# Optimization experiments

Hardware: AMD Instinct MI355X
Metric: run time of the kernel (lower is better)

## Reference

```python
import jax, jax.numpy as jnp
import numpy as np

N_SEEDS = 2500
N_JOINTS = 24
D_FEAT = 131


def setup_inputs() -> dict:
    key = jax.random.key(0)
    k1, k2, k3, k4, k5 = jax.random.split(key, 5)
    B = 256
    seed_features = jax.random.normal(k1, (B, N_SEEDS, D_FEAT), dtype=jnp.float32)
    # Conv1d kernel_size=1 weights == matrices over the channel dim
    s1 = 1.0 / np.sqrt(N_SEEDS)
    s2 = 1.0 / np.sqrt(N_JOINTS)
    W1 = jax.random.uniform(k2, (N_JOINTS, N_SEEDS), jnp.float32, -s1, s1)
    b1 = jax.random.uniform(k3, (N_JOINTS,), jnp.float32, -s1, s1)
    W2 = jax.random.uniform(k4, (N_JOINTS, N_JOINTS), jnp.float32, -s2, s2)
    b2 = jax.random.uniform(k5, (N_JOINTS,), jnp.float32, -s2, s2)
    return {"seed_features": seed_features, "W1": W1, "b1": b1, "W2": W2, "b2": b2}


def reference(seed_features, W1, b1, W2, b2):
    # conv1d(k=1) over channels: [B,2500,131] -> [B,24,131]
    h = jax.nn.relu(jnp.einsum('oc,bcl->bol', W1, seed_features) + b1[None, :, None])
    query = jnp.einsum('oc,bcl->bol', W2, h) + b2[None, :, None]        # [B,24,131]
    scores = jnp.einsum('bjl,bnl->bjn', query, seed_features)            # [B,24,2500]
    attention = jax.nn.softmax(scores, axis=-1)
    output = jnp.einsum('bjn,bnl->bjl', attention, seed_features)        # [B,24,131]
    return output, attention
```

## Files before the change

### kernel.cpp

```cpp
#include <hip/hip_runtime.h>
#include <cstdint>
#include <cstddef>

#define NB 256
#define NS 2500
#define NJ 24
#define DF 131

#define QSEG 4
#define TSEG 640

#define KP 2528
#define XROWS 2528
#define LPq 136
#define CSP 66
#define OSTRIDE ((size_t)NB * NJ * DF)

using short8 = __attribute__((ext_vector_type(8))) short;
using f32x4  = __attribute__((ext_vector_type(4))) float;

#define F_XN   0ull
#define F_W1B  176029696ull
#define F_QBF  176191488ull
#define F_PO   178419712ull
#define F_MD   191297536ull
#define F_P    191494144ull
#define WS_FULL 222558208ull

__device__ __forceinline__ unsigned short f2bf(float x) {
  union { float f; unsigned u; } v; v.f = x;
  unsigned r = v.u + 0x7fffu + ((v.u >> 16) & 1u);
  return (unsigned short)(r >> 16);
}
__device__ __forceinline__ float bf2f(unsigned us) {
  union { unsigned u; float f; } v; v.u = us << 16;
  return v.f;
}
__device__ __forceinline__ f32x4 mfma16(short8 a, short8 b, f32x4 c) {
  return __builtin_amdgcn_mfma_f32_16x16x32_bf16(a, b, c, 0, 0, 0);
}

__global__ __launch_bounds__(256) void kT2(const float* __restrict__ W1,
                                           unsigned short* __restrict__ W1b) {
  int dwi = blockIdx.x * 256 + threadIdx.x;
  if (dwi >= 32 * (KP / 2)) return;
  int row = dwi / (KP / 2);
  int kk = (dwi - row * (KP / 2)) * 2;
  unsigned lo = (row < NJ && kk     < NS) ? f2bf(W1[row * NS + kk])     : 0;
  unsigned hi = (row < NJ && kk + 1 < NS) ? f2bf(W1[row * NS + kk + 1]) : 0;
  ((unsigned*)W1b)[dwi] = lo | (hi << 16);
}

__global__ __launch_bounds__(256) void kPn(const float* __restrict__ sf,
                                           unsigned short* __restrict__ Xn) {
  int b = blockIdx.x / 20;
  int chunk = blockIdx.x - 20 * b;
  int c0 = chunk * 128;
  int w = threadIdx.x >> 6, lane = threadIdx.x & 63;
  const float* xb = sf + (size_t)b * (NS * DF);
  unsigned short* xnb = Xn + (size_t)b * ((size_t)XROWS * LPq);

#pragma unroll 4
  for (int i = 0; i < 32; ++i) {
    int r = w * 32 + i;
    int c = c0 + r;
    if (c >= XROWS) continue;
    bool vc = c < NS;
    const float* g = xb + (size_t)c * DF;
    float v0 = vc ? g[lane] : 0.f;
    float v1 = vc ? g[64 + lane] : 0.f;
    float v2 = (vc && lane < 3) ? g[128 + lane] : 0.f;
    unsigned short* d = xnb + (size_t)c * LPq;
    d[lane] = f2bf(v0);
    d[64 + lane] = f2bf(v1);
    if (lane < 8) d[128 + lane] = (lane < 3) ? f2bf(v2) : (unsigned short)0;
  }
}

__global__ __launch_bounds__(512) void kMM(const unsigned short* __restrict__ Xn,
                                           const unsigned short* __restrict__ A,
                                           int astride, int amax,
                                           float* __restrict__ Cp) {
  __shared__ unsigned short xs[144 * CSP];
  unsigned* xs4 = (unsigned*)xs;
  int b = blockIdx.x >> 2;
  int s = blockIdx.x & 3;
  int w = threadIdx.x >> 6, lane = threadIdx.x & 63;
  int lr = lane & 15, lg = lane >> 4;
  const unsigned* xb4 = (const unsigned*)(Xn + (size_t)b * ((size_t)XROWS * LPq));
  const unsigned short* Ab = A + (size_t)b * astride * KP;

  int nu = (w < 2) ? 3 : 2;
  f32x4 acc[3];
#pragma unroll
  for (int t = 0; t < 3; ++t) acc[t] = (f32x4){0.f, 0.f, 0.f, 0.f};

  int ch0 = s * 10;
  unsigned pre[9];
#pragma unroll
  for (int k = 0; k < 8; ++k)
    pre[k] = xb4[(size_t)(ch0 * 64 + w * 8 + k) * (LPq / 2) + lane];
  pre[8] = 0;
  if (lane < 32)
    pre[8] = xb4[(size_t)(ch0 * 64 + w * 8 + (lane >> 2)) * (LPq / 2) + 64 + (lane & 3)];

  for (int i = 0; i < 10; ++i) {
    int ch = ch0 + i;
    int c0 = ch * 64;
    int CS = (ch < 39) ? 64 : 32;
    __syncthreads();
#pragma unroll
    for (int k = 0; k < 8; ++k) {
      int r = w * 8 + k;
      if (r < CS) {
        xs[(2 * lane) * CSP + r]     = (unsigned short)(pre[k] & 0xffffu);
        xs[(2 * lane + 1) * CSP + r] = (unsigned short)(pre[k] >> 16);
      }
    }
    if (lane < 32) {
      int r = w * 8 + (lane >> 2);
      if (r < CS) {
        int l0 = 128 + 2 * (lane & 3);
        xs[l0 * CSP + r]       = (unsigned short)(pre[8] & 0xffffu);
        xs[(l0 + 1) * CSP + r] = (unsigned short)(pre[8] >> 16);
      }
    }
    __syncthreads();
    if (i + 1 < 10) {
      int c1 = c0 + 64;
      int CSn = (ch + 1 < 39) ? 64 : 32;
#pragma unroll
      for (int k = 0; k < 8; ++k) {
        int r = w * 8 + k;
        pre[k] = (r < CSn) ? xb4[(size_t)(c1 + r) * (LPq / 2) + lane] : 0u;
      }
      pre[8] = 0;
      if (lane < 32) {
        int r = w * 8 + (lane >> 2);
        if (r < CSn)
          pre[8] = xb4[(size_t)(c1 + r) * (LPq / 2) + 64 + (lane & 3)];
      }
    }
    int nks = CS >> 5;
    for (int ks = 0; ks < nks; ++ks) {
#pragma unroll
      for (int t = 0; t < 3; ++t) {
        if (t < nu) {
          int u = w + 8 * t;
          int m = u / 9, nt = u - 9 * m;
          int arow = m * 16 + lr; if (arow > amax) arow = amax;
          const unsigned short* ap = Ab + (size_t)arow * KP + c0 + ks * 32 + lg * 8;
          short8 av = *(const short8*)ap;
          int bb = (nt * 16 + lr) * (CSP / 2) + ks * 16 + lg * 4;
          unsigned b0 = xs4[bb], b1 = xs4[bb + 1], b2 = xs4[bb + 2], b3 = xs4[bb + 3];
          short8 bv;
          ((unsigned*)&bv)[0] = b0; ((unsigned*)&bv)[1] = b1;
          ((unsigned*)&bv)[2] = b2; ((unsigned*)&bv)[3] = b3;
          acc[t] = mfma16(av, bv, acc[t]);
        }
      }
    }
  }
  float* Cb = Cp + (size_t)(s * NB + b) * (NJ * DF);
#pragma unroll
  for (int t = 0; t < 3; ++t) {
    if (t < nu) {
      int u = w + 8 * t;
      int m = u / 9, nt = u - 9 * m;
      int lcol = nt * 16 + lr;
      if (lcol < DF) {
#pragma unroll
        for (int r = 0; r < 4; ++r) {
          int j = m * 16 + lg * 4 + r;
          if (j < NJ) Cb[(size_t)j * DF + lcol] = acc[t][r];
        }
      }
    }
  }
}

__global__ __launch_bounds__(512) void kR4(const float* __restrict__ po,
                                           float* __restrict__ out) {
  int i = blockIdx.x * 512 + threadIdx.x;
  out[i] = po[i] + po[OSTRIDE + i] + po[2 * OSTRIDE + i] + po[3 * OSTRIDE + i];
}

__global__ __launch_bounds__(512) void k1b(const float* __restrict__ po,
                                           const float* __restrict__ W2,
                                           const float* __restrict__ b1v,
                                           const float* __restrict__ b2v,
                                           unsigned short* __restrict__ qbf) {
  int flat = blockIdx.x * 512 + threadIdx.x;
  if (flat >= NB * LPq) return;
  int l = flat % LPq;
  int b = flat / LPq;
  unsigned short* qp = qbf + (size_t)b * (32 * LPq) + l;
  if (l >= DF) {
#pragma unroll
    for (int j = 0; j < 32; ++j) qp[j * LPq] = 0;
    return;
  }
  const float* p0 = po + (size_t)b * (NJ * DF) + l;
  float hv[NJ];
#pragma unroll
  for (int o = 0; o < NJ; ++o)
    hv[o] = fmaxf(b1v[o] + p0[o * DF] + p0[OSTRIDE + o * DF] +
                  p0[2 * OSTRIDE + o * DF] + p0[3 * OSTRIDE + o * DF], 0.f);
  float q[NJ];
  for (int o = 0; o < NJ; ++o) {
    float sv = b2v[o];
#pragma unroll
    for (int i = 0; i < NJ; ++i) sv = fmaf(W2[o * NJ + i], hv[i], sv);
    q[o] = sv;
  }
#pragma unroll
  for (int j = 0; j < NJ; ++j) qp[j * LPq] = f2bf(q[j]);
#pragma unroll
  for (int j = NJ; j < 32; ++j) qp[j * LPq] = 0;
}

__global__ __launch_bounds__(512) void k2m(const unsigned short* __restrict__ Xn,
                                           const unsigned short* __restrict__ qbf,
                                           unsigned short* __restrict__ P,
                                           float* __restrict__ md) {
  __shared__ float wm[8][24];
  __shared__ float wd[8][24];
  int b = blockIdx.x >> 2, seg = blockIdx.x & 3;
  int w = threadIdx.x >> 6, lane = threadIdx.x & 63;
  int lr = lane & 15, lg = lane >> 4;
  const short8 z8 = {0, 0, 0, 0, 0, 0, 0, 0};

  const unsigned short* qb = qbf + (size_t)b * (32 * LPq);
  short8 aq0[5], aq1[5];
#pragma unroll
  for (int ks = 0; ks < 4; ++ks) {
    aq0[ks] = *(const short8*)(qb + (size_t)lr * LPq + ks * 32 + lg * 8);
    aq1[ks] = *(const short8*)(qb + (size_t)(16 + lr) * LPq + ks * 32 + lg * 8);
  }
  aq0[4] = (lg == 0) ? *(const short8*)(qb + (size_t)lr * LPq + 128) : z8;
  aq1[4] = (lg == 0) ? *(const short8*)(qb + (size_t)(16 + lr) * LPq + 128) : z8;

  const unsigned short* xb = Xn + (size_t)b * ((size_t)XROWS * LPq);
  int ntl = (seg < 3) ? 40 : 37;

  f32x4 s0[5], s1[5];
  float m8[8];
#pragma unroll
  for (int r = 0; r < 8; ++r) m8[r] = -1e30f;

#pragma unroll
  for (int i = 0; i < 5; ++i) {
    s0[i] = (f32x4){0.f, 0.f, 0.f, 0.f};
    s1[i] = (f32x4){0.f, 0.f, 0.f, 0.f};
    int ti = w + 8 * i;
    if (ti < ntl) {
      int n = (seg * 40 + ti) * 16 + lr;
      const unsigned short* bp = xb + (size_t)n * LPq + lg * 8;
      short8 bx[5];
#pragma unroll
      for (int ks = 0; ks < 4; ++ks) bx[ks] = *(const short8*)(bp + ks * 32);
      bx[4] = (lg == 0) ? *(const short8*)(xb + (size_t)n * LPq + 128) : z8;
      f32x4 a0 = {0.f, 0.f, 0.f, 0.f}, a1 = {0.f, 0.f, 0.f, 0.f};
#pragma unroll
      for (int ks = 0; ks < 5; ++ks) {
        a0 = mfma16(aq0[ks], bx[ks], a0);
        a1 = mfma16(aq1[ks], bx[ks], a1);
      }
      s0[i] = a0; s1[i] = a1;
#pragma unroll
      for (int r = 0; r < 4; ++r) {
        m8[r]     = fmaxf(m8[r],     a0[r]);
        m8[4 + r] = fmaxf(m8[4 + r], a1[r]);
      }
    }
  }
#pragma unroll
  for (int r = 0; r < 8; ++r)
#pragma unroll
    for (int off = 1; off < 16; off <<= 1)
      m8[r] = fmaxf(m8[r], __shfl_xor(m8[r], off));
  if (lr == 0) {
#pragma unroll
    for (int r = 0; r < 4; ++r) {
      wm[w][lg * 4 + r] = m8[r];
      if (lg < 2) wm[w][16 + lg * 4 + r] = m8[4 + r];
    }
  }
  __syncthreads();
  float mseg[8];
#pragma unroll
  for (int r = 0; r < 4; ++r) {
    float m0 = wm[0][lg * 4 + r];
#pragma unroll
    for (int wv = 1; wv < 8; ++wv) m0 = fmaxf(m0, wm[wv][lg * 4 + r]);
    mseg[r] = m0;
    int j1 = 16 + (lg & 1) * 4 + r;
    float m1 = wm[0][j1];
#pragma unroll
    for (int wv = 1; wv < 8; ++wv) m1 = fmaxf(m1, wm[wv][j1]);
    mseg[4 + r] = m1;
  }
  float d8[8];
#pragma unroll
  for (int r = 0; r < 8; ++r) d8[r] = 0.f;
#pragma unroll
  for (int i = 0; i < 5; ++i) {
    int ti = w + 8 * i;
    if (ti < ntl) {
      int n = (seg * 40 + ti) * 16 + lr;
      bool valid = n < NS;
#pragma unroll
      for (int r = 0; r < 4; ++r) {
        float p0 = __expf(s0[i][r] - mseg[r]);
        float p1 = __expf(s1[i][r] - mseg[4 + r]);
        if (valid) {
          P[((size_t)b * NJ + lg * 4 + r) * KP + n] = f2bf(p0);
          d8[r] += p0;
          if (lg < 2) {
            P[((size_t)b * NJ + 16 + lg * 4 + r) * KP + n] = f2bf(p1);
            d8[4 + r] += p1;
          }
        }
      }
    }
  }
#pragma unroll
  for (int r = 0; r < 8; ++r)
#pragma unroll
    for (int off = 1; off < 16; off <<= 1)
      d8[r] += __shfl_xor(d8[r], off);
  if (lr == 0) {
#pragma unroll
    for (int r = 0; r < 4; ++r) {
      wd[w][lg * 4 + r] = d8[r];
      if (lg < 2) wd[w][16 + lg * 4 + r] = d8[4 + r];
    }
  }
  __syncthreads();
  if (threadIdx.x < NJ) {
    int j = threadIdx.x;
    float m = wm[0][j], d = 0.f;
#pragma unroll
    for (int wv = 1; wv < 8; ++wv) m = fmaxf(m, wm[wv][j]);
#pragma unroll
    for (int wv = 0; wv < 8; ++wv) d += wd[wv][j];
    float* mp = md + ((size_t)b * QSEG + seg) * 48;
    mp[j] = m;
    mp[24 + j] = d;
  }
}

__global__ __launch_bounds__(256) void kW(unsigned short* __restrict__ P,
                                          const float* __restrict__ md,
                                          float* __restrict__ attn) {
  int bj = blockIdx.x;
  int b = bj / NJ, j = bj - b * NJ;
  const float* mp = md + (size_t)b * (QSEG * 48);
  float ms[QSEG];
  float m = -1e30f;
#pragma unroll
  for (int s = 0; s < QSEG; ++s) { ms[s] = mp[s * 48 + j]; m = fmaxf(m, ms[s]); }
  float d = 0.f;
#pragma unroll
  for (int s = 0; s < QSEG; ++s) d += mp[s * 48 + 24 + j] * __expf(ms[s] - m);
  float rinv = 1.f / d;
  float cs[QSEG];
#pragma unroll
  for (int s = 0; s < QSEG; ++s) cs[s] = __expf(ms[s] - m) * rinv;

  unsigned* prow = (unsigned*)(P + (size_t)bj * KP);
  float2* arow = (float2*)(attn + (size_t)bj * NS);
  for (int i = threadIdx.x; i < NS / 2; i += 256) {
    unsigned pk = prow[i];
    int n0 = 2 * i;
    float p0 = bf2f(pk & 0xffffu) * cs[n0 / TSEG];
    float p1 = bf2f(pk >> 16) * cs[(n0 + 1) / TSEG];
    arow[i] = make_float2(p0, p1);
    prow[i] = (unsigned)f2bf(p0) | ((unsigned)f2bf(p1) << 16);
  }
  if (threadIdx.x < (KP - NS) / 2) prow[NS / 2 + threadIdx.x] = 0;
}

#define KSEG 8
#define CSEG 313
#define SEGN 625
#define TN 64
#define LDP 132
#define WS_W1T 0u
#define WS_QTF 60000u
#define WS_MDF (WS_QTF + 804864u)
#define WS_PHF (WS_MDF + (unsigned)(NB * QSEG * 48))
#define SEGSTRIDE ((size_t)NB * NJ * DF)

__global__ __launch_bounds__(256) void kT_f(const float* __restrict__ W1,
                                            float* __restrict__ W1t) {
  int i = blockIdx.x * 256 + threadIdx.x;
  if (i >= NJ * NS) return;
  int o = i / NS, c = i - o * NS;
  W1t[c * NJ + o] = W1[i];
}

__global__ __launch_bounds__(192) void kH_f(const float* __restrict__ sf,
                                            const float* __restrict__ W1t,
                                            float* __restrict__ ph) {
  int b = blockIdx.x >> 3;
  int s = blockIdx.x & 7;
  int l = threadIdx.x;
  int c0 = s * CSEG;
  int cnt = NS - c0; if (cnt > CSEG) cnt = CSEG;
  const float* xp = sf + (size_t)b * (NS * DF) + (size_t)c0 * DF;
  const float* wp = W1t + (size_t)c0 * NJ;
  float acc[NJ];
#pragma unroll
  for (int o = 0; o < NJ; ++o) acc[o] = 0.f;
  if (l < DF) {
#pragma unroll 2
    for (int c = 0; c < cnt; ++c) {
      float xv = xp[(size_t)c * DF + l];
#pragma unroll
      for (int o = 0; o < NJ; ++o) acc[o] = fmaf(wp[c * NJ + o], xv, acc[o]);
    }
    float* pp = ph + (size_t)(s * NB + b) * (NJ * DF) + l;
#pragma unroll
    for (int o = 0; o < NJ; ++o) pp[o * DF] = acc[o];
  }
}

__global__ __launch_bounds__(512) void k1b_f(const float* __restrict__ ph,
                                             const float* __restrict__ W2,
                                             const float* __restrict__ b1v,
                                             const float* __restrict__ b2v,
                                             float* __restrict__ q_t) {
  int flat = blockIdx.x * 512 + threadIdx.x;
  if (flat >= NB * DF) return;
  int l = flat % DF;
  int b = flat / DF;
  const float* p0 = ph + (size_t)(b * NJ) * DF + l;
  float hv[NJ];
#pragma unroll
  for (int o = 0; o < NJ; ++o) hv[o] = b1v[o];
  for (int s = 0; s < KSEG; ++s) {
#pragma unroll
    for (int o = 0; o < NJ; ++o) hv[o] += p0[s * SEGSTRIDE + o * DF];
  }
#pragma unroll
  for (int o = 0; o < NJ; ++o) hv[o] = fmaxf(hv[o], 0.f);
  float q[NJ];
  for (int o = 0; o < NJ; ++o) {
    float sv = b2v[o];
#pragma unroll
    for (int i = 0; i < NJ; ++i) sv = fmaf(W2[o * NJ + i], hv[i], sv);
    q[o] = sv;
  }
  float4* qp = (float4*)(q_t + (size_t)flat * NJ);
#pragma unroll
  for (int v = 0; v < 6; ++v)
    qp[v] = make_float4(q[4 * v], q[4 * v + 1], q[4 * v + 2], q[4 * v + 3]);
}

__global__ __launch_bounds__(256) void k2_f(const float* __restrict__ sf,
                                            const float* __restrict__ q_t,
                                            float* __restrict__ raw,
                                            float* __restrict__ md) {
  __shared__ __align__(16) float xs[TN * LDP];
  int b = blockIdx.x >> 2;
  int s = blockIdx.x & 3;
  int tid = threadIdx.x;
  int wid = tid >> 6, lane = tid & 63;
  int jq = __builtin_amdgcn_readfirstlane(wid);

  const float* sft = sf + (size_t)b * (NS * DF) + (size_t)(s * SEGN) * DF;
  const float* qb = q_t + (size_t)b * (DF * NJ) + jq * 6;
  float* rawb = raw + (size_t)b * (NJ * NS) + (size_t)(s * SEGN);

  float m6[6], d6[6];
#pragma unroll
  for (int i = 0; i < 6; ++i) { m6[i] = -1e30f; d6[i] = 0.f; }

  const int NT = (SEGN + TN - 1) / TN;
  for (int t = 0; t < NT; ++t) {
    int n0 = t * TN;
    int nmax = SEGN - n0; if (nmax > TN) nmax = TN;
    __syncthreads();
#pragma unroll
    for (int rr = 0; rr < 16; ++rr) {
      int r = wid * 16 + rr;
      if (r < nmax) {
        const float* g = sft + (size_t)(n0 + r) * DF;
        float* d = xs + r * LDP;
        d[lane] = g[lane];
        d[64 + lane] = g[64 + lane];
        if (lane < 3) d[128 + lane] = g[128 + lane];
      }
    }
    __syncthreads();
    if (lane < nmax) {
      const float* xrow = xs + lane * LDP;
      float sa[6];
#pragma unroll
      for (int i = 0; i < 6; ++i) sa[i] = 0.f;
      for (int l4 = 0; l4 < 32; ++l4) {
        float4 xv = *(const float4*)(xrow + 4 * l4);
        const float* q4 = qb + (4 * l4) * NJ;
#pragma unroll
        for (int i = 0; i < 6; ++i) sa[i] = fmaf(q4[i], xv.x, sa[i]);
#pragma unroll
        for (int i = 0; i < 6; ++i) sa[i] = fmaf(q4[NJ + i], xv.y, sa[i]);
#pragma unroll
        for (int i = 0; i < 6; ++i) sa[i] = fmaf(q4[2 * NJ + i], xv.z, sa[i]);
#pragma unroll
        for (int i = 0; i < 6; ++i) sa[i] = fmaf(q4[3 * NJ + i], xv.w, sa[i]);
      }
#pragma unroll
      for (int l = 128; l < DF; ++l) {
        float xv = xrow[l];
#pragma unroll
        for (int i = 0; i < 6; ++i) sa[i] = fmaf(qb[l * NJ + i], xv, sa[i]);
      }
      int nr = n0 + lane;
#pragma unroll
      for (int i = 0; i < 6; ++i) {
        rawb[(size_t)(jq * 6 + i) * NS + nr] = sa[i];
        float mn = fmaxf(m6[i], sa[i]);
        d6[i] = d6[i] * __expf(m6[i] - mn) + __expf(sa[i] - mn);
        m6[i] = mn;
      }
    }
  }
#pragma unroll
  for (int i = 0; i < 6; ++i) {
    float m = m6[i], d = d6[i];
    for (int off = 32; off > 0; off >>= 1) {
      float mo = __shfl_xor(m, off);
      float dd = __shfl_xor(d, off);
      float nm = fmaxf(m, mo);
      d = d * __expf(m - nm) + dd * __expf(mo - nm);
      m = nm;
    }
    m6[i] = m; d6[i] = d;
  }
  if (lane == 0) {
    float* mp = md + ((size_t)b * QSEG + s) * 48;
#pragma unroll
    for (int i = 0; i < 6; ++i) {
      mp[jq * 6 + i] = m6[i];
      mp[24 + jq * 6 + i] = d6[i];
    }
  }
}

__global__ __launch_bounds__(256) void k3_f(float* __restrict__ attn,
                                            const float* __restrict__ md) {
  int bj = blockIdx.x;
  int b = bj / NJ;
  int j = bj - b * NJ;
  const float* mp = md + (size_t)b * (QSEG * 48);
  float m = -1e30f, d = 0.f;
#pragma unroll
  for (int s = 0; s < QSEG; ++s) {
    float ms = mp[s * 48 + j], ds = mp[s * 48 + 24 + j];
    float nm = fmaxf(m, ms);
    d = d * __expf(m - nm) + ds * __expf(ms - nm);
    m = nm;
  }
  float r = 1.f / d;
  float* p = attn + (size_t)bj * NS;
  for (int n = threadIdx.x; n < NS; n += 256)
    p[n] = __expf(p[n] - m) * r;
}

__global__ __launch_bounds__(192) void k4_f(const float* __restrict__ sf,
                                            const float* __restrict__ attn,
                                            float* __restrict__ po) {
  int b = blockIdx.x >> 3;
  int s = blockIdx.x & 7;
  int l = threadIdx.x;
  int n0 = s * CSEG;
  int cnt = NS - n0; if (cnt > CSEG) cnt = CSEG;
  const float* xp = sf + (size_t)b * (NS * DF) + (size_t)n0 * DF;
  const float* ap = attn + (size_t)b * (NJ * NS) + n0;
  float acc[NJ];
#pragma unroll
  for (int o = 0; o < NJ; ++o) acc[o] = 0.f;
  if (l < DF) {
#pragma unroll 2
    for (int n = 0; n < cnt; ++n) {
      float xv = xp[(size_t)n * DF + l];
#pragma unroll
      for (int o = 0; o < NJ; ++o) acc[o] = fmaf(ap[(size_t)o * NS + n], xv, acc[o]);
    }
    float* pp = po + (size_t)(s * NB + b) * (NJ * DF) + l;
#pragma unroll
    for (int o = 0; o < NJ; ++o) pp[o * DF] = acc[o];
  }
}

__global__ __launch_bounds__(512) void k5_f(const float* __restrict__ po,
                                            float* __restrict__ out) {
  int i = blockIdx.x * 512 + threadIdx.x;
  float v = 0.f;
#pragma unroll
  for (int s = 0; s < KSEG; ++s) v += po[s * SEGSTRIDE + i];
  out[i] = v;
}

extern "C" void kernel_launch(void* const* d_in, const int* in_sizes, int n_in,
                              void* d_out, int out_size, void* d_ws, size_t ws_size,
                              hipStream_t stream) {
  const float* sf = (const float*)d_in[0];
  const float* W1 = (const float*)d_in[1];
  const float* b1 = (const float*)d_in[2];
  const float* W2 = (const float*)d_in[3];
  const float* b2 = (const float*)d_in[4];
  float* out = (float*)d_out;
  float* attn = out + (size_t)NB * NJ * DF;

  if (ws_size >= WS_FULL) {
    unsigned short* Xn  = (unsigned short*)((char*)d_ws + F_XN);
    unsigned short* W1b = (unsigned short*)((char*)d_ws + F_W1B);
    unsigned short* qbf = (unsigned short*)((char*)d_ws + F_QBF);
    float* po   = (float*)((char*)d_ws + F_PO);
    float* md   = (float*)((char*)d_ws + F_MD);
    unsigned short* P   = (unsigned short*)((char*)d_ws + F_P);

    kT2<<<158, 256, 0, stream>>>(W1, W1b);
    kPn<<<NB * 20, 256, 0, stream>>>(sf, Xn);
    kMM<<<NB * 4, 512, 0, stream>>>(Xn, W1b, 0, 31, po);
    k1b<<<68, 512, 0, stream>>>(po, W2, b1, b2, qbf);
    k2m<<<NB * QSEG, 512, 0, stream>>>(Xn, qbf, P, md);
    kW <<<NB * NJ, 256, 0, stream>>>(P, md, attn);
    kMM<<<NB * 4, 512, 0, stream>>>(Xn, P, NJ, 23, po);
    kR4<<<1572, 512, 0, stream>>>(po, out);
  } else {
    float* ws = (float*)d_ws;
    float* W1t = ws + WS_W1T;
    float* q_t = ws + WS_QTF;
    float* md  = ws + WS_MDF;
    float* ph  = ws + WS_PHF;
    kT_f <<<235, 256, 0, stream>>>(W1, W1t);
    kH_f <<<NB * KSEG, 192, 0, stream>>>(sf, W1t, ph);
    k1b_f<<<66, 512, 0, stream>>>(ph, W2, b1, b2, q_t);
    k2_f <<<NB * QSEG, 256, 0, stream>>>(sf, q_t, attn, md);
    k3_f <<<NB * NJ, 256, 0, stream>>>(attn, md);
    k4_f <<<NB * KSEG, 192, 0, stream>>>(sf, attn, ph);
    k5_f <<<1572, 512, 0, stream>>>(ph, out);
  }
}
```

Before: 357.3 us.

## Fuse bf16 conversion into first GEMM and defer softmax segment rescaling

Replaces the separate fp32-to-bf16 conversion kernel plus the first GEMM with one kernel. It reads the fp32 seed features, writes the bf16 copy for later stages, and stages tiles in shared memory for the MFMA GEMM, prefetching the next chunk into registers. The softmax-weight kernel no longer rewrites the rescaled probabilities back into P. Instead it stores per-segment scale factors that the final reduction applies to each partial output, so the second GEMM consumes the unnormalized bf16 probabilities. This saves a full pass over the input and a write pass over P, at the cost of a more complex fused kernel with less parallelism in the conversion step.

```diff
diff --git a/kernel.cpp b/kernel.cpp
--- a/kernel.cpp
+++ b/kernel.cpp
@@ -24,8 +24,9 @@
 #define F_QBF  176191488ull
 #define F_PO   178419712ull
 #define F_MD   191297536ull
-#define F_P    191494144ull
-#define WS_FULL 222558208ull
+#define F_CS   191494144ull
+#define F_P    191592448ull
+#define WS_FULL 222656512ull
 
 __device__ __forceinline__ unsigned short f2bf(float x) {
   union { float f; unsigned u; } v; v.f = x;
@@ -51,29 +52,126 @@
   ((unsigned*)W1b)[dwi] = lo | (hi << 16);
 }
 
-__global__ __launch_bounds__(256) void kPn(const float* __restrict__ sf,
-                                           unsigned short* __restrict__ Xn) {
-  int b = blockIdx.x / 20;
-  int chunk = blockIdx.x - 20 * b;
-  int c0 = chunk * 128;
+__global__ __launch_bounds__(512) void kMH(const float* __restrict__ sf,
+                                           const unsigned short* __restrict__ W1b,
+                                           unsigned short* __restrict__ Xn,
+                                           float* __restrict__ Cp) {
+  __shared__ unsigned short xs[144 * CSP];
+  unsigned* xs4 = (unsigned*)xs;
+  int b = blockIdx.x >> 2;
+  int s = blockIdx.x & 3;
   int w = threadIdx.x >> 6, lane = threadIdx.x & 63;
+  int lr = lane & 15, lg = lane >> 4;
   const float* xb = sf + (size_t)b * (NS * DF);
-  unsigned short* xnb = Xn + (size_t)b * ((size_t)XROWS * LPq);
-
-#pragma unroll 4
-  for (int i = 0; i < 32; ++i) {
-    int r = w * 32 + i;
-    int c = c0 + r;
-    if (c >= XROWS) continue;
+  unsigned* xnb4 = (unsigned*)(Xn + (size_t)b * ((size_t)XROWS * LPq));
+
+  int nu = (w < 2) ? 3 : 2;
+  f32x4 acc[3];
+#pragma unroll
+  for (int t = 0; t < 3; ++t) acc[t] = (f32x4){0.f, 0.f, 0.f, 0.f};
+
+  int ch0 = s * 10;
+  int q = lane & 3;
+  unsigned pre[9];
+#pragma unroll
+  for (int k = 0; k < 8; ++k) {
+    int c = ch0 * 64 + w * 8 + k;
     bool vc = c < NS;
-    const float* g = xb + (size_t)c * DF;
-    float v0 = vc ? g[lane] : 0.f;
-    float v1 = vc ? g[64 + lane] : 0.f;
-    float v2 = (vc && lane < 3) ? g[128 + lane] : 0.f;
-    unsigned short* d = xnb + (size_t)c * LPq;
-    d[lane] = f2bf(v0);
-    d[64 + lane] = f2bf(v1);
-    if (lane < 8) d[128 + lane] = (lane < 3) ? f2bf(v2) : (unsigned short)0;
+    float f0 = vc ? xb[(size_t)c * DF + 2 * lane] : 0.f;
+    float f1 = vc ? xb[(size_t)c * DF + 2 * lane + 1] : 0.f;
+    pre[k] = (unsigned)f2bf(f0) | ((unsigned)f2bf(f1) << 16);
+  }
+  pre[8] = 0;
+  if (lane < 32) {
+    int c = ch0 * 64 + w * 8 + (lane >> 2);
+    bool vc = c < NS;
+    int l0 = 128 + 2 * q;
+    float f0 = (vc && q < 2) ? xb[(size_t)c * DF + l0] : 0.f;
+    float f1 = (vc && q == 0) ? xb[(size_t)c * DF + 129] : 0.f;
+    pre[8] = (unsigned)f2bf(f0) | ((unsigned)f2bf(f1) << 16);
+  }
+
+  for (int i = 0; i < 10; ++i) {
+    int ch = ch0 + i;
+    int c0 = ch * 64;
+    int CS = (ch < 39) ? 64 : 32;
+    __syncthreads();
+#pragma unroll
+    for (int k = 0; k < 8; ++k) {
+      int r = w * 8 + k;
+      if (r < CS) {
+        xnb4[(size_t)(c0 + r) * (LPq / 2) + lane] = pre[k];
+        xs[(2 * lane) * CSP + r]     = (unsigned short)(pre[k] & 0xffffu);
+        xs[(2 * lane + 1) * CSP + r] = (unsigned short)(pre[k] >> 16);
+      }
+    }
+    if (lane < 32) {
+      int r = w * 8 + (lane >> 2);
+      if (r < CS) {
+        xnb4[(size_t)(c0 + r) * (LPq / 2) + 64 + q] = pre[8];
+        int l0 = 128 + 2 * q;
+        xs[l0 * CSP + r]       = (unsigned short)(pre[8] & 0xffffu);
+        xs[(l0 + 1) * CSP + r] = (unsigned short)(pre[8] >> 16);
+      }
+    }
+    __syncthreads();
+    if (i + 1 < 10) {
+      int c1 = c0 + 64;
+      int CSn = (ch + 1 < 39) ? 64 : 32;
+#pragma unroll
+      for (int k = 0; k < 8; ++k) {
+        int r = w * 8 + k;
+        int c = c1 + r;
+        bool vc = (r < CSn) && (c < NS);
+        float f0 = vc ? xb[(size_t)c * DF + 2 * lane] : 0.f;
+        float f1 = vc ? xb[(size_t)c * DF + 2 * lane + 1] : 0.f;
+        pre[k] = (r < CSn) ? ((unsigned)f2bf(f0) | ((unsigned)f2bf(f1) << 16)) : 0u;
+      }
+      pre[8] = 0;
+      if (lane < 32) {
+        int r = w * 8 + (lane >> 2);
+        int c = c1 + r;
+        bool vc = (r < CSn) && (c < NS);
+        float f0 = (vc && q < 2) ? xb[(size_t)c * DF + 128 + 2 * q] : 0.f;
+        float f1 = (vc && q == 0) ? xb[(size_t)c * DF + 129] : 0.f;
+        pre[8] = (unsigned)f2bf(f0) | ((unsigned)f2bf(f1) << 16);
+      }
+    }
+    int nks = CS >> 5;
+    for (int ks = 0; ks < nks; ++ks) {
+#pragma unroll
+      for (int t = 0; t < 3; ++t) {
+        if (t < nu) {
+          int u = w + 8 * t;
+          int m = u / 9, nt = u - 9 * m;
+          int arow = m * 16 + lr; if (arow > 31) arow = 31;
+          const unsigned short* ap = W1b + (size_t)arow * KP + c0 + ks * 32 + lg * 8;
+          short8 av = *(const short8*)ap;
+          int bb = (nt * 16 + lr) * (CSP / 2) + ks * 16 + lg * 4;
+          unsigned b0 = xs4[bb], b1 = xs4[bb + 1], b2 = xs4[bb + 2], b3 = xs4[bb + 3];
+          short8 bv;
+          ((unsigned*)&bv)[0] = b0; ((unsigned*)&bv)[1] = b1;
+          ((unsigned*)&bv)[2] = b2; ((unsigned*)&bv)[3] = b3;
+          acc[t] = mfma16(av, bv, acc[t]);
+        }
+      }
+    }
+  }
+  float* Cb = Cp + (size_t)(s * NB + b) * (NJ * DF);
+#pragma unroll
+  for (int t = 0; t < 3; ++t) {
+    if (t < nu) {
+      int u = w + 8 * t;
+      int m = u / 9, nt = u - 9 * m;
+      int lcol = nt * 16 + lr;
+      if (lcol < DF) {
+#pragma unroll
+        for (int r = 0; r < 4; ++r) {
+          int j = m * 16 + lg * 4 + r;
+          if (j < NJ) Cb[(size_t)j * DF + lcol] = acc[t][r];
+        }
+      }
+    }
   }
 }
 
@@ -180,9 +278,13 @@
 }
 
 __global__ __launch_bounds__(512) void kR4(const float* __restrict__ po,
+                                           const float* __restrict__ csb,
                                            float* __restrict__ out) {
   int i = blockIdx.x * 512 + threadIdx.x;
-  out[i] = po[i] + po[OSTRIDE + i] + po[2 * OSTRIDE + i] + po[3 * OSTRIDE + i];
+  int bj = i / DF;
+  const float* cs = csb + (size_t)bj * 4;
+  out[i] = cs[0] * po[i] + cs[1] * po[OSTRIDE + i] +
+           cs[2] * po[2 * OSTRIDE + i] + cs[3] * po[3 * OSTRIDE + i];
 }
 
 __global__ __launch_bounds__(512) void k1b(const float* __restrict__ po,
@@ -352,7 +454,8 @@
 
 __global__ __launch_bounds__(256) void kW(unsigned short* __restrict__ P,
                                           const float* __restrict__ md,
-                                          float* __restrict__ attn) {
+                                          float* __restrict__ attn,
+                                          float* __restrict__ csb) {
   int bj = blockIdx.x;
   int b = bj / NJ, j = bj - b * NJ;
   const float* mp = md + (size_t)b * (QSEG * 48);
@@ -367,6 +470,13 @@
   float cs[QSEG];
 #pragma unroll
   for (int s = 0; s < QSEG; ++s) cs[s] = __expf(ms[s] - m) * rinv;
+  if (threadIdx.x < QSEG) {
+    float v = cs[0];
+    if (threadIdx.x == 1) v = cs[1];
+    if (threadIdx.x == 2) v = cs[2];
+    if (threadIdx.x == 3) v = cs[3];
+    csb[(size_t)bj * QSEG + threadIdx.x] = v;
+  }
 
   unsigned* prow = (unsigned*)(P + (size_t)bj * KP);
   float2* arow = (float2*)(attn + (size_t)bj * NS);
@@ -376,7 +486,6 @@
     float p0 = bf2f(pk & 0xffffu) * cs[n0 / TSEG];
     float p1 = bf2f(pk >> 16) * cs[(n0 + 1) / TSEG];
     arow[i] = make_float2(p0, p1);
-    prow[i] = (unsigned)f2bf(p0) | ((unsigned)f2bf(p1) << 16);
   }
   if (threadIdx.x < (KP - NS) / 2) prow[NS / 2 + threadIdx.x] = 0;
 }
@@ -621,16 +730,16 @@
     unsigned short* qbf = (unsigned short*)((char*)d_ws + F_QBF);
     float* po   = (float*)((char*)d_ws + F_PO);
     float* md   = (float*)((char*)d_ws + F_MD);
+    float* csb  = (float*)((char*)d_ws + F_CS);
     unsigned short* P   = (unsigned short*)((char*)d_ws + F_P);
 
     kT2<<<158, 256, 0, stream>>>(W1, W1b);
-    kPn<<<NB * 20, 256, 0, stream>>>(sf, Xn);
-    kMM<<<NB * 4, 512, 0, stream>>>(Xn, W1b, 0, 31, po);
+    kMH<<<NB * 4, 512, 0, stream>>>(sf, W1b, Xn, po);
     k1b<<<68, 512, 0, stream>>>(po, W2, b1, b2, qbf);
     k2m<<<NB * QSEG, 512, 0, stream>>>(Xn, qbf, P, md);
-    kW <<<NB * NJ, 256, 0, stream>>>(P, md, attn);
+    kW <<<NB * NJ, 256, 0, stream>>>(P, md, attn, csb);
     kMM<<<NB * 4, 512, 0, stream>>>(Xn, P, NJ, 23, po);
-    kR4<<<1572, 512, 0, stream>>>(po, out);
+    kR4<<<1572, 512, 0, stream>>>(po, csb, out);
   } else {
     float* ws = (float*)d_ws;
     float* W1t = ws + WS_W1T;
```

New measurement: 364.8 us. +2.1%, slower.

## Defer softmax segment rescale to reduction and double-buffer LDS in kMM

Applied to the files above, without the earlier changes.

kW no longer rewrites the bf16 P matrix with normalized probabilities. Instead it stores the per-segment softmax correction factors, and kR4 applies them when summing the four K-segment partial outputs. This works because the kMM K-split matches the softmax segment size. It removes a full read-modify-write pass over P. kMM also gets a double-buffered LDS tile, so the next chunk is staged after compute and only one barrier per iteration is needed, at the cost of twice the shared memory.

```diff
diff --git a/kernel.cpp b/kernel.cpp
--- a/kernel.cpp
+++ b/kernel.cpp
@@ -24,8 +24,9 @@
 #define F_QBF  176191488ull
 #define F_PO   178419712ull
 #define F_MD   191297536ull
-#define F_P    191494144ull
-#define WS_FULL 222558208ull
+#define F_CS   191494144ull
+#define F_P    191592448ull
+#define WS_FULL 222656512ull
 
 __device__ __forceinline__ unsigned short f2bf(float x) {
   union { float f; unsigned u; } v; v.f = x;
@@ -81,8 +82,7 @@
                                            const unsigned short* __restrict__ A,
                                            int astride, int amax,
                                            float* __restrict__ Cp) {
-  __shared__ unsigned short xs[144 * CSP];
-  unsigned* xs4 = (unsigned*)xs;
+  __shared__ unsigned short xs[2][144 * CSP];
   int b = blockIdx.x >> 2;
   int s = blockIdx.x & 3;
   int w = threadIdx.x >> 6, lane = threadIdx.x & 63;
@@ -96,39 +96,37 @@
   for (int t = 0; t < 3; ++t) acc[t] = (f32x4){0.f, 0.f, 0.f, 0.f};
 
   int ch0 = s * 10;
+  int q = lane & 3;
   unsigned pre[9];
 #pragma unroll
   for (int k = 0; k < 8; ++k)
     pre[k] = xb4[(size_t)(ch0 * 64 + w * 8 + k) * (LPq / 2) + lane];
   pre[8] = 0;
   if (lane < 32)
-    pre[8] = xb4[(size_t)(ch0 * 64 + w * 8 + (lane >> 2)) * (LPq / 2) + 64 + (lane & 3)];
+    pre[8] = xb4[(size_t)(ch0 * 64 + w * 8 + (lane >> 2)) * (LPq / 2) + 64 + q];
+#pragma unroll
+  for (int k = 0; k < 8; ++k) {
+    int r = w * 8 + k;
+    xs[0][(2 * lane) * CSP + r]     = (unsigned short)(pre[k] & 0xffffu);
+    xs[0][(2 * lane + 1) * CSP + r] = (unsigned short)(pre[k] >> 16);
+  }
+  if (lane < 32) {
+    int r = w * 8 + (lane >> 2);
+    int l0 = 128 + 2 * q;
+    xs[0][l0 * CSP + r]       = (unsigned short)(pre[8] & 0xffffu);
+    xs[0][(l0 + 1) * CSP + r] = (unsigned short)(pre[8] >> 16);
+  }
 
   for (int i = 0; i < 10; ++i) {
     int ch = ch0 + i;
     int c0 = ch * 64;
     int CS = (ch < 39) ? 64 : 32;
+    int cur = i & 1;
     __syncthreads();
-#pragma unroll
-    for (int k = 0; k < 8; ++k) {
-      int r = w * 8 + k;
-      if (r < CS) {
-        xs[(2 * lane) * CSP + r]     = (unsigned short)(pre[k] & 0xffffu);
-        xs[(2 * lane + 1) * CSP + r] = (unsigned short)(pre[k] >> 16);
-      }
-    }
-    if (lane < 32) {
-      int r = w * 8 + (lane >> 2);
-      if (r < CS) {
-        int l0 = 128 + 2 * (lane & 3);
-        xs[l0 * CSP + r]       = (unsigned short)(pre[8] & 0xffffu);
-        xs[(l0 + 1) * CSP + r] = (unsigned short)(pre[8] >> 16);
-      }
-    }
-    __syncthreads();
+    int CSn = 0;
     if (i + 1 < 10) {
       int c1 = c0 + 64;
-      int CSn = (ch + 1 < 39) ? 64 : 32;
+      CSn = (ch + 1 < 39) ? 64 : 32;
 #pragma unroll
       for (int k = 0; k < 8; ++k) {
         int r = w * 8 + k;
@@ -138,9 +136,10 @@
       if (lane < 32) {
         int r = w * 8 + (lane >> 2);
         if (r < CSn)
-          pre[8] = xb4[(size_t)(c1 + r) * (LPq / 2) + 64 + (lane & 3)];
-      }
-    }
+          pre[8] = xb4[(size_t)(c1 + r) * (LPq / 2) + 64 + q];
+      }
+    }
+    const unsigned* xc4 = (const unsigned*)xs[cur];
     int nks = CS >> 5;
     for (int ks = 0; ks < nks; ++ks) {
 #pragma unroll
@@ -152,11 +151,30 @@
           const unsigned short* ap = Ab + (size_t)arow * KP + c0 + ks * 32 + lg * 8;
           short8 av = *(const short8*)ap;
           int bb = (nt * 16 + lr) * (CSP / 2) + ks * 16 + lg * 4;
-          unsigned b0 = xs4[bb], b1 = xs4[bb + 1], b2 = xs4[bb + 2], b3 = xs4[bb + 3];
+          unsigned b0 = xc4[bb], b1 = xc4[bb + 1], b2 = xc4[bb + 2], b3 = xc4[bb + 3];
           short8 bv;
           ((unsigned*)&bv)[0] = b0; ((unsigned*)&bv)[1] = b1;
           ((unsigned*)&bv)[2] = b2; ((unsigned*)&bv)[3] = b3;
           acc[t] = mfma16(av, bv, acc[t]);
+        }
+      }
+    }
+    if (i + 1 < 10) {
+      unsigned short* xn = xs[cur ^ 1];
+#pragma unroll
+      for (int k = 0; k < 8; ++k) {
+        int r = w * 8 + k;
+        if (r < CSn) {
+          xn[(2 * lane) * CSP + r]     = (unsigned short)(pre[k] & 0xffffu);
+          xn[(2 * lane + 1) * CSP + r] = (unsigned short)(pre[k] >> 16);
+        }
+      }
+      if (lane < 32) {
+        int r = w * 8 + (lane >> 2);
+        if (r < CSn) {
+          int l0 = 128 + 2 * q;
+          xn[l0 * CSP + r]       = (unsigned short)(pre[8] & 0xffffu);
+          xn[(l0 + 1) * CSP + r] = (unsigned short)(pre[8] >> 16);
         }
       }
     }
@@ -180,9 +198,13 @@
 }
 
 __global__ __launch_bounds__(512) void kR4(const float* __restrict__ po,
+                                           const float* __restrict__ csb,
                                            float* __restrict__ out) {
   int i = blockIdx.x * 512 + threadIdx.x;
-  out[i] = po[i] + po[OSTRIDE + i] + po[2 * OSTRIDE + i] + po[3 * OSTRIDE + i];
+  int bj = i / DF;
+  const float* cs = csb + (size_t)bj * 4;
+  out[i] = cs[0] * po[i] + cs[1] * po[OSTRIDE + i] +
+           cs[2] * po[2 * OSTRIDE + i] + cs[3] * po[3 * OSTRIDE + i];
 }
 
 __global__ __launch_bounds__(512) void k1b(const float* __restrict__ po,
@@ -352,7 +374,8 @@
 
 __global__ __launch_bounds__(256) void kW(unsigned short* __restrict__ P,
                                           const float* __restrict__ md,
-                                          float* __restrict__ attn) {
+                                          float* __restrict__ attn,
+                                          float* __restrict__ csb) {
   int bj = blockIdx.x;
   int b = bj / NJ, j = bj - b * NJ;
   const float* mp = md + (size_t)b * (QSEG * 48);
@@ -367,6 +390,13 @@
   float cs[QSEG];
 #pragma unroll
   for (int s = 0; s < QSEG; ++s) cs[s] = __expf(ms[s] - m) * rinv;
+  if (threadIdx.x < QSEG) {
+    float v = cs[0];
+    if (threadIdx.x == 1) v = cs[1];
+    if (threadIdx.x == 2) v = cs[2];
+    if (threadIdx.x == 3) v = cs[3];
+    csb[(size_t)bj * QSEG + threadIdx.x] = v;
+  }
 
   unsigned* prow = (unsigned*)(P + (size_t)bj * KP);
   float2* arow = (float2*)(attn + (size_t)bj * NS);
@@ -376,7 +406,6 @@
     float p0 = bf2f(pk & 0xffffu) * cs[n0 / TSEG];
     float p1 = bf2f(pk >> 16) * cs[(n0 + 1) / TSEG];
     arow[i] = make_float2(p0, p1);
-    prow[i] = (unsigned)f2bf(p0) | ((unsigned)f2bf(p1) << 16);
   }
   if (threadIdx.x < (KP - NS) / 2) prow[NS / 2 + threadIdx.x] = 0;
 }
@@ -621,6 +650,7 @@
     unsigned short* qbf = (unsigned short*)((char*)d_ws + F_QBF);
     float* po   = (float*)((char*)d_ws + F_PO);
     float* md   = (float*)((char*)d_ws + F_MD);
+    float* csb  = (float*)((char*)d_ws + F_CS);
     unsigned short* P   = (unsigned short*)((char*)d_ws + F_P);
 
     kT2<<<158, 256, 0, stream>>>(W1, W1b);
@@ -628,9 +658,9 @@
     kMM<<<NB * 4, 512, 0, stream>>>(Xn, W1b, 0, 31, po);
     k1b<<<68, 512, 0, stream>>>(po, W2, b1, b2, qbf);
     k2m<<<NB * QSEG, 512, 0, stream>>>(Xn, qbf, P, md);
-    kW <<<NB * NJ, 256, 0, stream>>>(P, md, attn);
+    kW <<<NB * NJ, 256, 0, stream>>>(P, md, attn, csb);
     kMM<<<NB * 4, 512, 0, stream>>>(Xn, P, NJ, 23, po);
-    kR4<<<1572, 512, 0, stream>>>(po, out);
+    kR4<<<1572, 512, 0, stream>>>(po, csb, out);
   } else {
     float* ws = (float*)d_ws;
     float* W1t = ws + WS_W1T;
```

Measured after the change: 319.0 us, median of 3. 1.12x faster.
